# Kernel optimization log

Hardware: AMD Instinct MI355X
Metric: run time of the kernel (lower is better)

Reference implementation:

```python
import jax, jax.numpy as jnp
import numpy as np

DT = 1.0
EPS = 1e-6


def setup_inputs() -> dict:
    key = jax.random.key(0)
    k1, k2, k3, k4 = jax.random.split(key, 4)
    batch, in_ch, out_ch, state_dim, T = 16, 256, 256, 256, 8192
    u = jax.random.normal(k1, (batch, in_ch, T), dtype=jnp.float32)
    raw_lambda = jax.random.normal(k2, (state_dim,), dtype=jnp.float32)
    B_c = jax.random.normal(k3, (in_ch, state_dim), dtype=jnp.float32) * (1.0 / in_ch ** 0.5)
    C = jax.random.normal(k4, (state_dim, out_ch), dtype=jnp.float32) * (1.0 / state_dim ** 0.5)
    return {"u": u, "raw_lambda": raw_lambda, "B_c": B_c, "C": C}


def reference(u, raw_lambda, B_c, C):
    # ZOH discretization of diagonal SSM (all-real here since raw_lambda is real)
    lam = -jax.nn.softplus(raw_lambda)                 # (N,)
    A_d = jnp.exp(lam * DT)                            # (N,)
    factor = jnp.where(jnp.abs(lam) > EPS, (A_d - 1.0) / lam, jnp.full_like(lam, DT))
    B_d = B_c * factor[None, :]                        # (in_ch, N)

    # Precompute driving inputs for every step in one big GEMM: (T, B, N)
    x = jnp.einsum('bct,cn->tbn', u, B_d)

    batch, state_dim = u.shape[0], raw_lambda.shape[0]

    def step(s, x_t):
        s = s * A_d[None, :] + x_t                     # diagonal recurrence
        return s, s

    s0 = jnp.zeros((batch, state_dim), dtype=u.dtype)
    _, states = jax.lax.scan(step, s0, x)              # states: (T, B, N)

    # Project all states at once: y (B, out_ch, T)
    y = jnp.einsum('tbn,no->bot', states, C)
    return y
```

## Files before the change

kernel.cpp:

```cpp
#include <hip/hip_runtime.h>
#include <math.h>

typedef __attribute__((ext_vector_type(8)))  short short8;
typedef __attribute__((ext_vector_type(16))) float f32x16;

#define B_  16
#define C_  256
#define N_  256
#define O_  256
#define T_  8192
#define L_  64
#define NC_ 128

#define GLL16(gptr, lptr) \
  __builtin_amdgcn_global_load_lds((const __attribute__((address_space(1))) void*)(gptr), \
                                   (__attribute__((address_space(3))) void*)(lptr), 16, 0, 0)

__device__ inline unsigned short f2bf(float x) {
    unsigned u = __float_as_uint(x);
    u += 0x7fff + ((u >> 16) & 1);
    return (unsigned short)(u >> 16);
}
__device__ inline float bf2f(unsigned short h) {
    return __uint_as_float(((unsigned)h) << 16);
}
__device__ inline f32x16 zero16() {
    f32x16 z;
    #pragma unroll
    for (int i = 0; i < 16; ++i) z[i] = 0.f;
    return z;
}

__global__ __launch_bounds__(256) void k_prep(
    const float* __restrict__ raw_lambda, const float* __restrict__ B_c,
    const float* __restrict__ Cmat,
    float* __restrict__ Ad, float* __restrict__ AL,
    unsigned short* __restrict__ BdKf, unsigned short* __restrict__ CKf)
{
    const int r = blockIdx.x;
    const int t = threadIdx.x;
    const int kk = r >> 5, ri = r & 31;
    const int s = ri >> 4, hi = (ri >> 3) & 1, j = ri & 7;
    const int nt = t >> 5, l = (hi << 5) | (t & 31);
    const int idx = (((kk * 8 + nt) * 2 + s) * 64 + l) * 8 + j;

    if (blockIdx.y == 0) {
        const float x  = raw_lambda[t];
        const float sp = (x > 20.f) ? x : log1pf(expf(x));
        const float lam = -sp;
        const float ad  = expf(lam);
        const float factor = (fabsf(lam) > 1e-6f) ? (ad - 1.f) / lam : 1.f;
        if (r == 0) {
            Ad[t] = ad;
            float al = ad;
            #pragma unroll
            for (int i = 0; i < 6; ++i) al *= al;
            AL[t] = al;
        }
        BdKf[idx] = f2bf(B_c[r * N_ + t] * factor);
    } else {
        CKf[idx] = f2bf(Cmat[r * O_ + t]);
    }
}

__global__ __launch_bounds__(256) void k_phaseA(
    const float* __restrict__ u, const unsigned short* __restrict__ BdKf,
    const float* __restrict__ Ad, float* __restrict__ p_last,
    unsigned short* __restrict__ X, int doX)
{
    __shared__ __align__(16) unsigned short ut[16896];
    __shared__ __align__(16) unsigned short bb[2][8192];

    const int k = blockIdx.x, b = blockIdx.y;
    const int tid = threadIdx.x;
    const int w = tid >> 6, l = tid & 63, lo = l & 31, hi = l >> 5;
    const int t0 = k * L_;
    const float* ub = u + (size_t)b * C_ * T_ + t0;

    const float adq0 = Ad[(2 * w + 0) * 32 + lo];
    const float adq1 = Ad[(2 * w + 1) * 32 + lo];

    auto stage_bb = [&](int kk, int buf) {
        const char* src = (const char*)(BdKf + kk * 8192);
        #pragma unroll
        for (int q = 0; q < 4; ++q)
            GLL16(src + q * 4096 + w * 1024 + (l << 4),
                  (char*)bb[buf] + q * 4096 + w * 1024);
    };

    stage_bb(0, 0);

    float4 v[16];
    #pragma unroll
    for (int q = 0; q < 16; ++q) {
        const int i = q * 256 + tid, cl = i >> 4, t4 = i & 15;
        v[q] = *(const float4*)(ub + (size_t)cl * T_ + t4 * 4);
    }
    {
        unsigned* ud = (unsigned*)ut;
        #pragma unroll
        for (int q = 0; q < 16; ++q) {
            const int i = q * 256 + tid, cl = i >> 4, t4 = i & 15;
            float4 a = v[q], p;
            p.x = __shfl_xor(a.x, 16); p.y = __shfl_xor(a.y, 16);
            p.z = __shfl_xor(a.z, 16); p.w = __shfl_xor(a.w, 16);
            const bool odd = (cl & 1) != 0;
            const float l0 = odd ? p.z : a.x, h0 = odd ? a.z : p.x;
            const float l1 = odd ? p.w : a.y, h1 = odd ? a.w : p.y;
            const int r0 = odd ? 2 : 0;
            const int nb = cl >> 3, jd = (cl >> 1) & 3;
            const int tA = 4 * t4 + r0, tB = tA + 1;
            const int xsw = (tA >> 3) & 3;
            ud[tA * 132 + (((nb ^ xsw) << 2) | jd)] =
                f2bf(l0) | ((unsigned)f2bf(h0) << 16);
            ud[tB * 132 + (((nb ^ xsw) << 2) | jd)] =
                f2bf(l1) | ((unsigned)f2bf(h1) << 16);
        }
    }
    __syncthreads();

    f32x16 a00 = zero16(), a01 = zero16(), a10 = zero16(), a11 = zero16();
    #pragma unroll
    for (int kk = 0; kk < 8; ++kk) {
        const int cur = kk & 1;
        if (kk < 7) stage_bb(kk + 1, cur ^ 1);
        #pragma unroll
        for (int s = 0; s < 2; ++s) {
            const int blk8 = kk * 4 + s * 2 + hi;
            short8 fa0, fa1;
            { const int t = lo;
              fa0 = *(const short8*)(ut + t * 264 + ((blk8 ^ ((t >> 3) & 3)) << 3)); }
            { const int t = 32 + lo;
              fa1 = *(const short8*)(ut + t * 264 + ((blk8 ^ ((t >> 3) & 3)) << 3)); }
            const short8 fb0 = *(const short8*)(bb[cur] + (((2 * w + 0) * 2 + s) * 64 + l) * 8);
            const short8 fb1 = *(const short8*)(bb[cur] + (((2 * w + 1) * 2 + s) * 64 + l) * 8);
            a00 = __builtin_amdgcn_mfma_f32_32x32x16_bf16(fa0, fb0, a00, 0, 0, 0);
            a01 = __builtin_amdgcn_mfma_f32_32x32x16_bf16(fa0, fb1, a01, 0, 0, 0);
            a10 = __builtin_amdgcn_mfma_f32_32x32x16_bf16(fa1, fb0, a10, 0, 0, 0);
            a11 = __builtin_amdgcn_mfma_f32_32x32x16_bf16(fa1, fb1, a11, 0, 0, 0);
        }
        __syncthreads();
    }

    if (doX) {
        unsigned* Xd = (unsigned*)X + (size_t)(k * B_ + b) * 8192;
        #pragma unroll
        for (int f = 0; f < 4; ++f) {
            const f32x16 a = (f == 0) ? a00 : (f == 1) ? a01 : (f == 2) ? a10 : a11;
            unsigned dw[8];
            #pragma unroll
            for (int d = 0; d < 8; ++d)
                dw[d] = f2bf(a[2 * d]) | ((unsigned)f2bf(a[2 * d + 1]) << 16);
            unsigned* base = Xd + w * 2048 + f * 512 + l * 4;
            *(int4*)(base)       = *(const int4*)&dw[0];
            *(int4*)(base + 256) = *(const int4*)&dw[4];
        }
    }

    {
        float p[2];
        #pragma unroll
        for (int q = 0; q < 2; ++q) {
            const float ad = q ? adq1 : adq0;
            const float ad2 = ad * ad, ad4 = ad2 * ad2, ad8 = ad4 * ad4;
            const float ad16 = ad8 * ad8, ad32 = ad16 * ad16;
            float full[2];
            #pragma unroll
            for (int tt = 0; tt < 2; ++tt) {
                const f32x16 a = (tt == 0) ? (q == 0 ? a00 : a01)
                                           : (q == 0 ? a10 : a11);
                float v2[4];
                #pragma unroll
                for (int g = 0; g < 4; ++g)
                    v2[g] = fmaf(fmaf(fmaf(a[4*g], ad, a[4*g+1]), ad, a[4*g+2]), ad, a[4*g+3]);
                const float H = fmaf(fmaf(fmaf(v2[0], ad8, v2[1]), ad8, v2[2]), ad8, v2[3]);
                float P = hi ? H : H * ad4;
                P += __shfl_xor(P, 32);
                full[tt] = P;
            }
            p[q] = fmaf(full[0], ad32, full[1]);
        }
        if (hi == 0) {
            float* dst = p_last + (size_t)(k * B_ + b) * N_;
            dst[(2 * w + 0) * 32 + lo] = p[0];
            dst[(2 * w + 1) * 32 + lo] = p[1];
        }
    }
}

__global__ __launch_bounds__(256) void k_phaseB(
    const float* __restrict__ p_last, const float* __restrict__ AL,
    float* __restrict__ carry)
{
    __shared__ float buf[32 * 256];
    const int b = blockIdx.x, n = threadIdx.x;
    const float al = AL[n];
    float cur = 0.f;
    for (int kc = 0; kc < 4; ++kc) {
        __syncthreads();
        #pragma unroll
        for (int q = 0; q < 32; ++q)
            buf[q * 256 + n] = p_last[((size_t)(kc * 32 + q) * B_ + b) * N_ + n];
        __syncthreads();
        #pragma unroll
        for (int q = 0; q < 32; ++q) {
            carry[((size_t)(kc * 32 + q) * B_ + b) * N_ + n] = cur;
            cur = fmaf(cur, al, buf[q * 256 + n]);
        }
    }
}

__global__ __launch_bounds__(256) void k_phaseC(
    const unsigned short* __restrict__ X, const unsigned short* __restrict__ CKf,
    const float* __restrict__ Ad, const float* __restrict__ carry,
    float* __restrict__ y)
{
    __shared__ __align__(16) unsigned short xs[16896];
    __shared__ __align__(16) unsigned short bb[2][8192];

    const int k = blockIdx.x, b = blockIdx.y;
    const int tid = threadIdx.x;
    const int w = tid >> 6, l = tid & 63, lo = l & 31, hi = l >> 5;
    const int t0 = k * L_;

    auto stage_bb = [&](int kk, int buf) {
        const char* src = (const char*)(CKf + kk * 8192);
        #pragma unroll
        for (int q = 0; q < 4; ++q)
            GLL16(src + q * 4096 + w * 1024 + (l << 4),
                  (char*)bb[buf] + q * 4096 + w * 1024);
    };

    stage_bb(0, 0);
    {
        const char* src = (const char*)X + (size_t)(k * B_ + b) * 32768;
        #pragma unroll
        for (int q = 0; q < 8; ++q)
            GLL16(src + q * 4096 + w * 1024 + (l << 4),
                  (char*)xs + q * 4096 + w * 1024);
    }
    const float cv = carry[(size_t)(k * B_ + b) * N_ + tid];
    const float ad = Ad[tid];
    __syncthreads();

    unsigned arr[2][2][8];
    {
        const unsigned* xd = (const unsigned*)xs;
        const int w2 = tid >> 6, q2 = (tid >> 5) & 1, lo2 = tid & 31;
        #pragma unroll
        for (int tt = 0; tt < 2; ++tt)
            #pragma unroll
            for (int h2 = 0; h2 < 2; ++h2) {
                const unsigned* p = xd + w2 * 2048 + (tt * 2 + q2) * 512
                                       + (h2 * 32 + lo2) * 4;
                *(int4*)&arr[tt][h2][0] = *(const int4*)(p);
                *(int4*)&arr[tt][h2][4] = *(const int4*)(p + 256);
            }
    }
    __syncthreads();

    {
        const int nb = tid >> 3, nl = tid & 7;
        float s = cv;
        #pragma unroll
        for (int tt = 0; tt < 2; ++tt)
            #pragma unroll
            for (int g = 0; g < 4; ++g)
                #pragma unroll
                for (int h2 = 0; h2 < 2; ++h2) {
                    const unsigned d0 = arr[tt][h2][2 * g];
                    const unsigned d1 = arr[tt][h2][2 * g + 1];
                    const int tb = tt * 32 + 8 * g + 4 * h2;
                    const int swz = (((nb ^ ((tb >> 3) & 3)) << 3) | nl);
                    s = fmaf(s, ad, bf2f((unsigned short)(d0 & 0xffff)));
                    xs[(tb + 0) * 264 + swz] = f2bf(s);
                    s = fmaf(s, ad, bf2f((unsigned short)(d0 >> 16)));
                    xs[(tb + 1) * 264 + swz] = f2bf(s);
                    s = fmaf(s, ad, bf2f((unsigned short)(d1 & 0xffff)));
                    xs[(tb + 2) * 264 + swz] = f2bf(s);
                    s = fmaf(s, ad, bf2f((unsigned short)(d1 >> 16)));
                    xs[(tb + 3) * 264 + swz] = f2bf(s);
                }
    }
    __syncthreads();

    f32x16 c00 = zero16(), c01 = zero16(), c10 = zero16(), c11 = zero16();
    #pragma unroll
    for (int kk = 0; kk < 8; ++kk) {
        const int cur = kk & 1;
        if (kk < 7) stage_bb(kk + 1, cur ^ 1);
        #pragma unroll
        for (int s = 0; s < 2; ++s) {
            short8 fa[2];
            #pragma unroll
            for (int tt = 0; tt < 2; ++tt) {
                const int t = tt * 32 + lo;
                const int blk = (kk * 4 + s * 2 + hi) ^ ((t >> 3) & 3);
                fa[tt] = *(const short8*)(xs + t * 264 + blk * 8);
            }
            const short8 fb0 = *(const short8*)(bb[cur] + (((2 * w + 0) * 2 + s) * 64 + l) * 8);
            const short8 fb1 = *(const short8*)(bb[cur] + (((2 * w + 1) * 2 + s) * 64 + l) * 8);
            c00 = __builtin_amdgcn_mfma_f32_32x32x16_bf16(fa[0], fb0, c00, 0, 0, 0);
            c01 = __builtin_amdgcn_mfma_f32_32x32x16_bf16(fa[0], fb1, c01, 0, 0, 0);
            c10 = __builtin_amdgcn_mfma_f32_32x32x16_bf16(fa[1], fb0, c10, 0, 0, 0);
            c11 = __builtin_amdgcn_mfma_f32_32x32x16_bf16(fa[1], fb1, c11, 0, 0, 0);
        }
        __syncthreads();
    }

    #pragma unroll
    for (int tt = 0; tt < 2; ++tt)
        #pragma unroll
        for (int q = 0; q < 2; ++q) {
            const f32x16 a = (tt == 0) ? (q == 0 ? c00 : c01) : (q == 0 ? c10 : c11);
            const int o = (2 * w + q) * 32 + lo;
            float* yo = y + ((size_t)b * O_ + o) * T_ + t0 + tt * 32 + hi * 4;
            #pragma unroll
            for (int g = 0; g < 4; ++g) {
                float4 v;
                v.x = a[g * 4 + 0]; v.y = a[g * 4 + 1];
                v.z = a[g * 4 + 2]; v.w = a[g * 4 + 3];
                *(float4*)(yo + g * 8) = v;
            }
        }
}

__device__ __forceinline__ void gemm1_rc(
    const float* __restrict__ u, const unsigned short* __restrict__ BdKf,
    int b, int k, unsigned short* xs, unsigned short* ut, unsigned short* bb)
{
    const int tid = threadIdx.x;
    const int w = tid >> 6, l = tid & 63, lo = l & 31, hi = l >> 5;
    const int t0 = k * L_;
    f32x16 a00 = zero16(), a01 = zero16(), a10 = zero16(), a11 = zero16();
    for (int kk = 0; kk < 8; ++kk) {
        #pragma unroll
        for (int q = 0; q < 2; ++q) {
            const int i = q * 256 + tid, cl = i >> 4, t4 = i & 15;
            const float4 v = *(const float4*)(
                u + ((size_t)b * C_ + kk * 32 + cl) * T_ + t0 + t4 * 4);
            ut[(t4 * 4 + 0) * 40 + cl] = f2bf(v.x);
            ut[(t4 * 4 + 1) * 40 + cl] = f2bf(v.y);
            ut[(t4 * 4 + 2) * 40 + cl] = f2bf(v.z);
            ut[(t4 * 4 + 3) * 40 + cl] = f2bf(v.w);
        }
        {
            const unsigned short* src = BdKf + kk * 8192;
            #pragma unroll
            for (int q = 0; q < 4; ++q) {
                const int i16 = q * 256 + tid;
                *(int4*)(bb + i16 * 8) = *(const int4*)(src + i16 * 8);
            }
        }
        __syncthreads();
        #pragma unroll
        for (int s = 0; s < 2; ++s) {
            const short8 fa0 = *(const short8*)(ut + (0 * 32 + lo) * 40 + s * 16 + hi * 8);
            const short8 fa1 = *(const short8*)(ut + (1 * 32 + lo) * 40 + s * 16 + hi * 8);
            const short8 fb0 = *(const short8*)(bb + (((2 * w + 0) * 2 + s) * 64 + l) * 8);
            const short8 fb1 = *(const short8*)(bb + (((2 * w + 1) * 2 + s) * 64 + l) * 8);
            a00 = __builtin_amdgcn_mfma_f32_32x32x16_bf16(fa0, fb0, a00, 0, 0, 0);
            a01 = __builtin_amdgcn_mfma_f32_32x32x16_bf16(fa0, fb1, a01, 0, 0, 0);
            a10 = __builtin_amdgcn_mfma_f32_32x32x16_bf16(fa1, fb0, a10, 0, 0, 0);
            a11 = __builtin_amdgcn_mfma_f32_32x32x16_bf16(fa1, fb1, a11, 0, 0, 0);
        }
        __syncthreads();
    }
    #pragma unroll
    for (int tt = 0; tt < 2; ++tt)
        #pragma unroll
        for (int q = 0; q < 2; ++q) {
            const f32x16 a = (tt == 0) ? (q == 0 ? a00 : a01) : (q == 0 ? a10 : a11);
            const int n = (2 * w + q) * 32 + lo;
            #pragma unroll
            for (int g = 0; g < 4; ++g)
                #pragma unroll
                for (int p = 0; p < 2; ++p)
                    *(unsigned*)(xs + n * 66 + tt * 32 + hi * 4 + g * 8 + p * 2)
                        = f2bf(a[g * 4 + 2 * p]) | ((unsigned)f2bf(a[g * 4 + 2 * p + 1]) << 16);
        }
    __syncthreads();
}

__global__ __launch_bounds__(256) void k_phaseC_rc(
    const float* __restrict__ u, const unsigned short* __restrict__ BdKf,
    const unsigned short* __restrict__ CKf, const float* __restrict__ Ad,
    const float* __restrict__ carry, float* __restrict__ y)
{
    __shared__ __align__(16) unsigned short xs[16896];
    __shared__ __align__(16) unsigned short ut[2560];
    __shared__ __align__(16) unsigned short bb[8192];

    const int k = blockIdx.x, b = blockIdx.y;
    const int tid = threadIdx.x;
    const int w = tid >> 6, l = tid & 63, lo = l & 31, hi = l >> 5;
    const int t0 = k * L_;

    gemm1_rc(u, BdKf, b, k, xs, ut, bb);

    {
        const float a = Ad[tid];
        float s = carry[((size_t)k * B_ + b) * N_ + tid];
        float st[64];
        #pragma unroll
        for (int m = 0; m < 32; ++m) {
            const unsigned dw = *(const unsigned*)(xs + tid * 66 + 2 * m);
            s = fmaf(s, a, bf2f((unsigned short)(dw & 0xffff)));  st[2 * m] = s;
            s = fmaf(s, a, bf2f((unsigned short)(dw >> 16)));     st[2 * m + 1] = s;
        }
        __syncthreads();
        #pragma unroll
        for (int t = 0; t < 64; ++t) xs[t * 264 + tid] = f2bf(st[t]);
    }
    __syncthreads();

    f32x16 c00 = zero16(), c01 = zero16(), c10 = zero16(), c11 = zero16();
    for (int kk = 0; kk < 8; ++kk) {
        __syncthreads();
        {
            const unsigned short* src = CKf + kk * 8192;
            #pragma unroll
            for (int q = 0; q < 4; ++q) {
                const int i16 = q * 256 + tid;
                *(int4*)(bb + i16 * 8) = *(const int4*)(src + i16 * 8);
            }
        }
        __syncthreads();
        #pragma unroll
        for (int s = 0; s < 2; ++s) {
            const short8 fa0 = *(const short8*)(xs + (0 * 32 + lo) * 264 + kk * 32 + s * 16 + hi * 8);
            const short8 fa1 = *(const short8*)(xs + (1 * 32 + lo) * 264 + kk * 32 + s * 16 + hi * 8);
            const short8 fb0 = *(const short8*)(bb + (((2 * w + 0) * 2 + s) * 64 + l) * 8);
            const short8 fb1 = *(const short8*)(bb + (((2 * w + 1) * 2 + s) * 64 + l) * 8);
            c00 = __builtin_amdgcn_mfma_f32_32x32x16_bf16(fa0, fb0, c00, 0, 0, 0);
            c01 = __builtin_amdgcn_mfma_f32_32x32x16_bf16(fa0, fb1, c01, 0, 0, 0);
            c10 = __builtin_amdgcn_mfma_f32_32x32x16_bf16(fa1, fb0, c10, 0, 0, 0);
            c11 = __builtin_amdgcn_mfma_f32_32x32x16_bf16(fa1, fb1, c11, 0, 0, 0);
        }
    }

    #pragma unroll
    for (int tt = 0; tt < 2; ++tt)
        #pragma unroll
        for (int q = 0; q < 2; ++q) {
            const f32x16 a = (tt == 0) ? (q == 0 ? c00 : c01) : (q == 0 ? c10 : c11);
            const int o = (2 * w + q) * 32 + lo;
            float* yo = y + ((size_t)b * O_ + o) * T_ + t0 + tt * 32 + hi * 4;
            #pragma unroll
            for (int g = 0; g < 4; ++g) {
                float4 v;
                v.x = a[g * 4 + 0]; v.y = a[g * 4 + 1];
                v.z = a[g * 4 + 2]; v.w = a[g * 4 + 3];
                *(float4*)(yo + g * 8) = v;
            }
        }
}

extern "C" void kernel_launch(void* const* d_in, const int* in_sizes, int n_in,
                              void* d_out, int out_size, void* d_ws, size_t ws_size,
                              hipStream_t stream)
{
    const float* u  = (const float*)d_in[0];
    const float* rl = (const float*)d_in[1];
    const float* Bc = (const float*)d_in[2];
    const float* Cm = (const float*)d_in[3];
    float* y  = (float*)d_out;
    char*  ws = (char*)d_ws;

    float* Ad     = (float*)(ws + 0);
    float* AL     = (float*)(ws + 1024);
    float* p_last = (float*)(ws + 2048);
    float* carry  = (float*)(ws + 2048 + 2097152);
    unsigned short* BdKf = (unsigned short*)(ws + 2048 + 2 * 2097152);
    unsigned short* CKf  = (unsigned short*)(ws + 2048 + 2 * 2097152 + 131072);
    unsigned short* X    = (unsigned short*)(ws + 2048 + 2 * 2097152 + 2 * 131072);
    const size_t need = 2048 + 2ull * 2097152 + 2ull * 131072
                      + (size_t)NC_ * B_ * 32768;
    const int doX = (ws_size >= need) ? 1 : 0;

    k_prep  <<<dim3(256, 2),  dim3(256), 0, stream>>>(rl, Bc, Cm, Ad, AL, BdKf, CKf);
    k_phaseA<<<dim3(NC_, B_), dim3(256), 0, stream>>>(u, BdKf, Ad, p_last, X, doX);
    k_phaseB<<<dim3(B_),      dim3(256), 0, stream>>>(p_last, AL, carry);
    if (doX)
        k_phaseC<<<dim3(NC_, B_), dim3(256), 0, stream>>>(X, CKf, Ad, carry, y);
    else
        k_phaseC_rc<<<dim3(NC_, B_), dim3(256), 0, stream>>>(u, BdKf, CKf, Ad, carry, y);
}
```

Measured before the change: 122.6 us.

## Load weight fragments straight to registers with 3-deep prefetch, drop LDS staging

```diff
diff --git a/kernel.cpp b/kernel.cpp
--- a/kernel.cpp
+++ b/kernel.cpp
@@ -23,6 +23,11 @@
 }
 __device__ inline float bf2f(unsigned short h) {
     return __uint_as_float(((unsigned)h) << 16);
+}
+__device__ inline unsigned cvtpk(float a, float b) {
+    unsigned r;
+    asm("v_cvt_pk_bf16_f32 %0, %1, %2" : "=v"(r) : "v"(a), "v"(b));
+    return r;
 }
 __device__ inline f32x16 zero16() {
     f32x16 z;
@@ -63,32 +68,28 @@
     }
 }
 
-__global__ __launch_bounds__(256) void k_phaseA(
+#define LDFRAG(MAT, kk, buf) { \
+    _Pragma("unroll") \
+    for (int q_ = 0; q_ < 2; ++q_) \
+        _Pragma("unroll") \
+        for (int s_ = 0; s_ < 2; ++s_) \
+            fb[buf][q_ * 2 + s_] = *(const short8*)( \
+                (MAT) + ((((kk) * 8 + 2 * w + q_) * 2 + s_) * 64 + l) * 8); }
+
+__global__ __launch_bounds__(256, 2) void k_phaseA(
     const float* __restrict__ u, const unsigned short* __restrict__ BdKf,
     const float* __restrict__ Ad, float* __restrict__ p_last,
     unsigned short* __restrict__ X, int doX)
 {
     __shared__ __align__(16) unsigned short ut[16896];
-    __shared__ __align__(16) unsigned short bb[2][8192];
 
     const int k = blockIdx.x, b = blockIdx.y;
     const int tid = threadIdx.x;
     const int w = tid >> 6, l = tid & 63, lo = l & 31, hi = l >> 5;
-    const int t0 = k * L_;
-    const float* ub = u + (size_t)b * C_ * T_ + t0;
+    const float* ub = u + (size_t)b * C_ * T_ + k * L_;
 
     const float adq0 = Ad[(2 * w + 0) * 32 + lo];
     const float adq1 = Ad[(2 * w + 1) * 32 + lo];
-
-    auto stage_bb = [&](int kk, int buf) {
-        const char* src = (const char*)(BdKf + kk * 8192);
-        #pragma unroll
-        for (int q = 0; q < 4; ++q)
-            GLL16(src + q * 4096 + w * 1024 + (l << 4),
-                  (char*)bb[buf] + q * 4096 + w * 1024);
-    };
-
-    stage_bb(0, 0);
 
     float4 v[16];
     #pragma unroll
@@ -111,35 +112,32 @@
             const int nb = cl >> 3, jd = (cl >> 1) & 3;
             const int tA = 4 * t4 + r0, tB = tA + 1;
             const int xsw = (tA >> 3) & 3;
-            ud[tA * 132 + (((nb ^ xsw) << 2) | jd)] =
-                f2bf(l0) | ((unsigned)f2bf(h0) << 16);
-            ud[tB * 132 + (((nb ^ xsw) << 2) | jd)] =
-                f2bf(l1) | ((unsigned)f2bf(h1) << 16);
+            ud[tA * 132 + (((nb ^ xsw) << 2) | jd)] = cvtpk(l0, h0);
+            ud[tB * 132 + (((nb ^ xsw) << 2) | jd)] = cvtpk(l1, h1);
         }
     }
     __syncthreads();
 
     f32x16 a00 = zero16(), a01 = zero16(), a10 = zero16(), a11 = zero16();
+    short8 fb[3][4];
+    LDFRAG(BdKf, 0, 0)
+    LDFRAG(BdKf, 1, 1)
     #pragma unroll
     for (int kk = 0; kk < 8; ++kk) {
-        const int cur = kk & 1;
-        if (kk < 7) stage_bb(kk + 1, cur ^ 1);
+        if (kk < 6) LDFRAG(BdKf, kk + 2, (kk + 2) % 3)
         #pragma unroll
         for (int s = 0; s < 2; ++s) {
             const int blk8 = kk * 4 + s * 2 + hi;
-            short8 fa0, fa1;
-            { const int t = lo;
-              fa0 = *(const short8*)(ut + t * 264 + ((blk8 ^ ((t >> 3) & 3)) << 3)); }
-            { const int t = 32 + lo;
-              fa1 = *(const short8*)(ut + t * 264 + ((blk8 ^ ((t >> 3) & 3)) << 3)); }
-            const short8 fb0 = *(const short8*)(bb[cur] + (((2 * w + 0) * 2 + s) * 64 + l) * 8);
-            const short8 fb1 = *(const short8*)(bb[cur] + (((2 * w + 1) * 2 + s) * 64 + l) * 8);
+            const int tA2 = lo, tB2 = 32 + lo;
+            const short8 fa0 = *(const short8*)(ut + tA2 * 264 + ((blk8 ^ ((tA2 >> 3) & 3)) << 3));
+            const short8 fa1 = *(const short8*)(ut + tB2 * 264 + ((blk8 ^ ((tB2 >> 3) & 3)) << 3));
+            const short8 fb0 = fb[kk % 3][0 * 2 + s];
+            const short8 fb1 = fb[kk % 3][1 * 2 + s];
             a00 = __builtin_amdgcn_mfma_f32_32x32x16_bf16(fa0, fb0, a00, 0, 0, 0);
             a01 = __builtin_amdgcn_mfma_f32_32x32x16_bf16(fa0, fb1, a01, 0, 0, 0);
             a10 = __builtin_amdgcn_mfma_f32_32x32x16_bf16(fa1, fb0, a10, 0, 0, 0);
             a11 = __builtin_amdgcn_mfma_f32_32x32x16_bf16(fa1, fb1, a11, 0, 0, 0);
         }
-        __syncthreads();
     }
 
     if (doX) {
@@ -150,7 +148,7 @@
             unsigned dw[8];
             #pragma unroll
             for (int d = 0; d < 8; ++d)
-                dw[d] = f2bf(a[2 * d]) | ((unsigned)f2bf(a[2 * d + 1]) << 16);
+                dw[d] = cvtpk(a[2 * d], a[2 * d + 1]);
             unsigned* base = Xd + w * 2048 + f * 512 + l * 4;
             *(int4*)(base)       = *(const int4*)&dw[0];
             *(int4*)(base + 256) = *(const int4*)&dw[4];
@@ -210,28 +208,18 @@
     }
 }
 
-__global__ __launch_bounds__(256) void k_phaseC(
+__global__ __launch_bounds__(256, 2) void k_phaseC(
     const unsigned short* __restrict__ X, const unsigned short* __restrict__ CKf,
     const float* __restrict__ Ad, const float* __restrict__ carry,
     float* __restrict__ y)
 {
     __shared__ __align__(16) unsigned short xs[16896];
-    __shared__ __align__(16) unsigned short bb[2][8192];
 
     const int k = blockIdx.x, b = blockIdx.y;
     const int tid = threadIdx.x;
     const int w = tid >> 6, l = tid & 63, lo = l & 31, hi = l >> 5;
     const int t0 = k * L_;
 
-    auto stage_bb = [&](int kk, int buf) {
-        const char* src = (const char*)(CKf + kk * 8192);
-        #pragma unroll
-        for (int q = 0; q < 4; ++q)
-            GLL16(src + q * 4096 + w * 1024 + (l << 4),
-                  (char*)bb[buf] + q * 4096 + w * 1024);
-    };
-
-    stage_bb(0, 0);
     {
         const char* src = (const char*)X + (size_t)(k * B_ + b) * 32768;
         #pragma unroll
@@ -285,10 +273,12 @@
     __syncthreads();
 
     f32x16 c00 = zero16(), c01 = zero16(), c10 = zero16(), c11 = zero16();
+    short8 fb[3][4];
+    LDFRAG(CKf, 0, 0)
+    LDFRAG(CKf, 1, 1)
     #pragma unroll
     for (int kk = 0; kk < 8; ++kk) {
-        const int cur = kk & 1;
-        if (kk < 7) stage_bb(kk + 1, cur ^ 1);
+        if (kk < 6) LDFRAG(CKf, kk + 2, (kk + 2) % 3)
         #pragma unroll
         for (int s = 0; s < 2; ++s) {
             short8 fa[2];
@@ -298,14 +288,13 @@
                 const int blk = (kk * 4 + s * 2 + hi) ^ ((t >> 3) & 3);
                 fa[tt] = *(const short8*)(xs + t * 264 + blk * 8);
             }
-            const short8 fb0 = *(const short8*)(bb[cur] + (((2 * w + 0) * 2 + s) * 64 + l) * 8);
-            const short8 fb1 = *(const short8*)(bb[cur] + (((2 * w + 1) * 2 + s) * 64 + l) * 8);
+            const short8 fb0 = fb[kk % 3][0 * 2 + s];
+            const short8 fb1 = fb[kk % 3][1 * 2 + s];
             c00 = __builtin_amdgcn_mfma_f32_32x32x16_bf16(fa[0], fb0, c00, 0, 0, 0);
             c01 = __builtin_amdgcn_mfma_f32_32x32x16_bf16(fa[0], fb1, c01, 0, 0, 0);
             c10 = __builtin_amdgcn_mfma_f32_32x32x16_bf16(fa[1], fb0, c10, 0, 0, 0);
             c11 = __builtin_amdgcn_mfma_f32_32x32x16_bf16(fa[1], fb1, c11, 0, 0, 0);
         }
-        __syncthreads();
     }
 
     #pragma unroll
@@ -317,10 +306,10 @@
             float* yo = y + ((size_t)b * O_ + o) * T_ + t0 + tt * 32 + hi * 4;
             #pragma unroll
             for (int g = 0; g < 4; ++g) {
-                float4 v;
-                v.x = a[g * 4 + 0]; v.y = a[g * 4 + 1];
-                v.z = a[g * 4 + 2]; v.w = a[g * 4 + 3];
-                *(float4*)(yo + g * 8) = v;
+                float4 vv;
+                vv.x = a[g * 4 + 0]; vv.y = a[g * 4 + 1];
+                vv.z = a[g * 4 + 2]; vv.w = a[g * 4 + 3];
+                *(float4*)(yo + g * 8) = vv;
             }
         }
 }
@@ -448,10 +437,10 @@
             float* yo = y + ((size_t)b * O_ + o) * T_ + t0 + tt * 32 + hi * 4;
             #pragma unroll
             for (int g = 0; g < 4; ++g) {
-                float4 v;
-                v.x = a[g * 4 + 0]; v.y = a[g * 4 + 1];
-                v.z = a[g * 4 + 2]; v.w = a[g * 4 + 3];
-                *(float4*)(yo + g * 8) = v;
+                float4 vv;
+                vv.x = a[g * 4 + 0]; vv.y = a[g * 4 + 1];
+                vv.z = a[g * 4 + 2]; vv.w = a[g * 4 + 3];
+                *(float4*)(yo + g * 8) = vv;
             }
         }
 }
```

After: 107.5 us. -12.3%, faster.
